# Performance work log

Measured on AMD Instinct MI355X. Metric: run time of the kernel, lower is better.

The kernel has to match this reference:

```python
import jax, jax.numpy as jnp
import numpy as np


def setup_inputs() -> dict:
    key = jax.random.key(0)
    ks = jax.random.split(key, 8)
    N, D, G, H = 131072, 128, 2048, 512
    features = jax.random.normal(ks[0], (N, D), dtype=jnp.float32)
    graph_index = jnp.sort(jax.random.randint(ks[1], (N,), 0, G))
    s1 = 1.0 / np.sqrt(D)
    W_m = jax.random.uniform(ks[2], (H, D), jnp.float32, -s1, s1)
    b_m = jax.random.uniform(ks[3], (H,), jnp.float32, -s1, s1)
    s2 = 1.0 / np.sqrt(H)
    W_ih = jax.random.uniform(ks[4], (4 * H, 2 * H), jnp.float32, -s2, s2)
    W_hh = jax.random.uniform(ks[5], (4 * H, H), jnp.float32, -s2, s2)
    b_ih = jax.random.uniform(ks[6], (4 * H,), jnp.float32, -s2, s2)
    b_hh = jax.random.uniform(ks[7], (4 * H,), jnp.float32, -s2, s2)
    return dict(features=features, graph_index=graph_index, W_m=W_m, b_m=b_m,
                W_ih=W_ih, W_hh=W_hh, b_ih=b_ih, b_hh=b_hh, num_graphs=G)


def reference(features, graph_index, W_m, b_m, W_ih, W_hh, b_ih, b_hh, num_graphs):
    H = W_m.shape[0]
    LOOP = 3
    EPS = 1e-7
    NEG_BIG = -1e10
    m = features @ W_m.T + b_m                      # [N, H]
    h = jnp.zeros((num_graphs, H), m.dtype)
    c = jnp.zeros((num_graphs, H), m.dtype)
    q_star = jnp.zeros((num_graphs, 2 * H), m.dtype)
    for _ in range(LOOP):
        # PyTorch LSTMCell: gates in (i, f, g, o) order
        gates = q_star @ W_ih.T + h @ W_hh.T + (b_ih + b_hh)   # [G, 4H]
        i_g, f_g, g_g, o_g = jnp.split(gates, 4, axis=-1)
        c = jax.nn.sigmoid(f_g) * c + jax.nn.sigmoid(i_g) * jnp.tanh(g_g)
        h = jax.nn.sigmoid(o_g) * jnp.tanh(c)
        # attention scores per node against its graph's query h
        e = jnp.sum(m * h[graph_index], axis=-1, keepdims=True)  # [N, 1]
        e_max = jax.ops.segment_max(e, graph_index, num_segments=num_graphs)
        e_max = jax.lax.stop_gradient(
            jnp.where(jnp.isfinite(e_max), e_max, NEG_BIG))
        e = e - e_max[graph_index]
        exp_e = jnp.exp(jnp.clip(e, -30.0, 20.0))
        exp_sum = jax.ops.segment_sum(exp_e, graph_index, num_segments=num_graphs)
        a = exp_e / (exp_sum[graph_index] + EPS)                 # [N, 1]
        r = jax.ops.segment_sum(m * a, graph_index, num_segments=num_graphs)  # [G, H]
        q_star = jnp.concatenate([h, r], axis=-1)                # [G, 2H]
    return q_star
```

## Files before the change

kernel.cpp:

```cpp
#include <hip/hip_runtime.h>

#define N_NODES 131072
#define DIM     128
#define NG      2048
#define HD      512

typedef unsigned short u16;
typedef _Float16 half8 __attribute__((ext_vector_type(8)));
typedef float  f32x4  __attribute__((ext_vector_type(4)));

__device__ u16   g_wm[(size_t)HD * DIM];
__device__ u16   g_wmT[(size_t)DIM * HD];
__device__ u16   g_wgf[(size_t)2048 * 640];
__device__ u16   g_wih2[(size_t)2048 * 512];
__device__ float g_bc[2048];
__device__ float g_bf[2048];
__device__ float g_gh[2048];
__device__ float g_c0[512];
__device__ float g_w20[128];
__device__ float g_w2[(size_t)NG * DIM];
__device__ float g_tp[NG];
__device__ u16   g_Acat[(size_t)NG * 640];
__device__ u16   g_h3[(size_t)NG * HD];
__device__ float g_c[(size_t)NG * HD];
__device__ int   g_start[NG + 1];
__device__ int   g_isbf16;
__device__ int   g_idx64;

__device__ __forceinline__ float bf2f(u16 u) {
  unsigned v = ((unsigned)u) << 16;
  float f; __builtin_memcpy(&f, &v, 4); return f;
}
__device__ __forceinline__ float u2f_hi(unsigned u) {
  unsigned v = u & 0xFFFF0000u;
  float f; __builtin_memcpy(&f, &v, 4); return f;
}
__device__ __forceinline__ float u2f_lo(unsigned u) {
  unsigned v = u << 16;
  float f; __builtin_memcpy(&f, &v, 4); return f;
}
__device__ __forceinline__ u16 f2bf(float f) {
  unsigned u; __builtin_memcpy(&u, &f, 4);
  u += 0x7FFFu + ((u >> 16) & 1u);
  return (u16)(u >> 16);
}
__device__ __forceinline__ u16 f2h(float f) {
  _Float16 h = (_Float16)f; u16 u; __builtin_memcpy(&u, &h, 2); return u;
}
__device__ __forceinline__ float h2f(u16 u) {
  _Float16 h; __builtin_memcpy(&h, &u, 2); return (float)h;
}
__device__ __forceinline__ float rdf(const void* p, int i) {
  return g_isbf16 ? bf2f(((const u16*)p)[i]) : ((const float*)p)[i];
}
__device__ __forceinline__ float rdl(const void* p, int i, int isb) {
  return isb ? bf2f(((const u16*)p)[i]) : ((const float*)p)[i];
}

#define GLD16(gp, lp) __builtin_amdgcn_global_load_lds(                          \
    (const __attribute__((address_space(1))) void*)(gp),                         \
    (__attribute__((address_space(3))) void*)(lp), 16, 0, 0)

#define NWP ((size_t)HD * DIM / 2)
#define NWT ((size_t)DIM * HD / 2)
#define NW1 ((size_t)2048 * 512 / 2)
#define NW2 ((size_t)2048 * 512 / 2)
#define W_PAIRS (NWP + NWT + NW1 + NW2)

__global__ __launch_bounds__(256) void k_s0(const void* feat, const void* gidxv,
                                            const void* wmp, const void* wih,
                                            const void* whh) {
  __shared__ int s_cnt;
  const int t = threadIdx.x;
  if (t == 0) s_cnt = 0;
  __syncthreads();
  {
    u16 u = ((const u16*)feat)[t];
    float v = bf2f(u);
    float a = fabsf(v);
    int ok = (v == v) && a >= 1e-6f && a <= 1e6f;
    atomicAdd(&s_cnt, ok);
  }
  __syncthreads();
  const int isb = (s_cnt >= 230);
  const int idx64 = (((const int*)gidxv)[N_NODES - 1] == 0);
  if (blockIdx.x == 0 && t == 0) { g_isbf16 = isb; g_idx64 = idx64; }

  for (size_t i = (size_t)blockIdx.x * 256 + t; i < W_PAIRS;
       i += (size_t)gridDim.x * 256) {
    if (i < NWP) {
      float v0, v1;
      if (isb) {
        unsigned pr = ((const unsigned*)wmp)[i];
        v0 = bf2f((u16)pr); v1 = bf2f((u16)(pr >> 16));
      } else {
        float2 v = ((const float2*)wmp)[i];
        v0 = v.x; v1 = v.y;
      }
      ((unsigned*)g_wm)[i] = (unsigned)f2h(v0) | ((unsigned)f2h(v1) << 16);
    } else if (i < NWP + NWT) {
      size_t p = i - NWP;
      int d = (int)(p >> 8), j = (int)(p & 255) * 2;
      float v0 = rdl(wmp, j * DIM + d, isb);
      float v1 = rdl(wmp, (j + 1) * DIM + d, isb);
      ((unsigned*)g_wmT)[(size_t)d * 256 + (j >> 1)] =
          (unsigned)f2h(v0) | ((unsigned)f2h(v1) << 16);
    } else if (i < NWP + NWT + NW1) {
      size_t p = i - NWP - NWT;
      int n = (int)(p >> 8), kp = (int)(p & 255), k = kp * 2;
      int orig = (n & 3) * 512 + (n >> 2);
      float v0 = rdl(wih, orig * 1024 + k, isb)     + rdl(whh, orig * 512 + k, isb);
      float v1 = rdl(wih, orig * 1024 + k + 1, isb) + rdl(whh, orig * 512 + k + 1, isb);
      ((unsigned*)g_wgf)[(size_t)n * 320 + kp] =
          (unsigned)f2h(v0) | ((unsigned)f2h(v1) << 16);
    } else {
      size_t p = i - NWP - NWT - NW1;
      int n = (int)(p >> 8), kp = (int)(p & 255), k = kp * 2;
      int orig = (n & 3) * 512 + (n >> 2);
      float v0 = rdl(wih, orig * 1024 + 512 + k, isb);
      float v1 = rdl(wih, orig * 1024 + 512 + k + 1, isb);
      ((unsigned*)g_wih2)[(size_t)n * 256 + kp] =
          (unsigned)f2h(v0) | ((unsigned)f2h(v1) << 16);
    }
  }
  if (blockIdx.x < 512) {
    int n = blockIdx.x * 256 + t;
    int gg = idx64 ? (int)((const long long*)gidxv)[n] : ((const int*)gidxv)[n];
    if (n == 0) {
      for (int x = 0; x <= gg; ++x) g_start[x] = 0;
    } else {
      int gp = idx64 ? (int)((const long long*)gidxv)[n - 1] : ((const int*)gidxv)[n - 1];
      for (int x = gp + 1; x <= gg; ++x) g_start[x] = n;
    }
    if (n == N_NODES - 1) {
      for (int x = gg + 1; x <= NG; ++x) g_start[x] = N_NODES;
    }
  }
}

__global__ __launch_bounds__(256) void k_s1(const void* bih, const void* bhh,
                                            const void* bm) {
  alignas(16) __shared__ char smem[16384];
  const int t = threadIdx.x, b = blockIdx.x;
  if (b < 128) {
    float* s_bm = (float*)smem;
    float* s_h0 = s_bm + 512;
    for (int p = t; p < 512; p += 256) {
      s_bm[p] = rdf(bm, p);
      float xi = rdf(bih, p)        + rdf(bhh, p);
      float xg = rdf(bih, p + 1024) + rdf(bhh, p + 1024);
      float xo = rdf(bih, p + 1536) + rdf(bhh, p + 1536);
      float si = 1.f / (1.f + __expf(-xi));
      float tg = tanhf(xg);
      float so = 1.f / (1.f + __expf(-xo));
      s_h0[p] = so * tanhf(si * tg);
    }
    __syncthreads();
    const int rloc = t >> 4, k = t & 15;
    const int n = b * 16 + rloc;
    float sbf = 0.f, sgh = 0.f;
#pragma unroll
    for (int j = 0; j < 4; ++j) {
      const int e = k * 8 + j * 128;
      half8 w2v = *(const half8*)(g_wih2 + (size_t)n * 512 + e);
      half8 w1v = *(const half8*)(g_wgf  + (size_t)n * 640 + e);
#pragma unroll
      for (int d = 0; d < 8; ++d) {
        sbf += (float)w2v[d] * s_bm[e + d];
        sgh += (float)w1v[d] * s_h0[e + d];
      }
    }
#pragma unroll
    for (int o = 1; o < 16; o <<= 1) {
      sbf += __shfl_xor(sbf, o, 64);
      sgh += __shfl_xor(sgh, o, 64);
    }
    if (k == 0) {
      const int orig = (n & 3) * 512 + (n >> 2);
      g_bf[n] = sbf;
      g_gh[n] = sgh;
      g_bc[n] = rdf(bih, orig) + rdf(bhh, orig);
    }
  } else if (b < 192) {
    u16* As = (u16*)smem;
    u16* Bs = As + 4096;
    const int bx = b - 128;
    const int lid = t & 63, w = t >> 6;
    const int m0 = (bx & 31) * 64, n0 = (bx >> 5) * 64;
    const int rr = lid & 15, quad = lid >> 4;
    const int rsub = lid >> 3;
    const int cs = (lid & 7) ^ rsub;
    const int wm = (w >> 1) * 32, wn = (w & 1) * 32;
    f32x4 acc[2][2] = {};
    for (int kt = 0; kt < 8; ++kt) {
      const int k0 = kt * 64;
      GLD16(g_wih2 + (size_t)(m0 + w * 16 + rsub) * 512 + k0 + cs * 8, As + (w * 16) * 64);
      GLD16(g_wih2 + (size_t)(m0 + w * 16 + 8 + rsub) * 512 + k0 + cs * 8, As + (w * 16 + 8) * 64);
      GLD16(g_wmT + (size_t)(n0 + w * 16 + rsub) * 512 + k0 + cs * 8, Bs + (w * 16) * 64);
      GLD16(g_wmT + (size_t)(n0 + w * 16 + 8 + rsub) * 512 + k0 + cs * 8, Bs + (w * 16 + 8) * 64);
      __syncthreads();
#pragma unroll
      for (int kk = 0; kk < 2; ++kk) {
        const int qb = kk * 4 + quad;
        const int sw = (qb ^ (rr & 7)) << 3;
        half8 af[2], bfr[2];
#pragma unroll
        for (int i = 0; i < 2; ++i) af[i]  = *(const half8*)(As + (wm + i * 16 + rr) * 64 + sw);
#pragma unroll
        for (int j = 0; j < 2; ++j) bfr[j] = *(const half8*)(Bs + (wn + j * 16 + rr) * 64 + sw);
#pragma unroll
        for (int i = 0; i < 2; ++i)
#pragma unroll
          for (int j = 0; j < 2; ++j)
            acc[i][j] = __builtin_amdgcn_mfma_f32_16x16x32_f16(bfr[j], af[i], acc[i][j], 0, 0, 0);
      }
      __syncthreads();
    }
#pragma unroll
    for (int i = 0; i < 2; ++i)
#pragma unroll
      for (int j = 0; j < 2; ++j) {
        const int row = m0 + wm + i * 16 + rr;
        const int c0 = n0 + wn + j * 16 + quad * 4;
        u16 h4[4];
#pragma unroll
        for (int r = 0; r < 4; ++r) h4[r] = f2h(acc[i][j][r]);
        *(uint2*)(g_wgf + (size_t)row * 640 + 512 + c0) =
            make_uint2((unsigned)h4[0] | ((unsigned)h4[1] << 16),
                       (unsigned)h4[2] | ((unsigned)h4[3] << 16));
      }
  } else if (b == 192) {
    float* s_h   = (float*)smem;
    float* s_red = s_h + 512;
    for (int j = t; j < 512; j += 256) {
      float xi = rdf(bih, j)        + rdf(bhh, j);
      float xg = rdf(bih, j + 1024) + rdf(bhh, j + 1024);
      float xo = rdf(bih, j + 1536) + rdf(bhh, j + 1536);
      float si = 1.f / (1.f + __expf(-xi));
      float tg = tanhf(xg);
      float so = 1.f / (1.f + __expf(-xo));
      float cn = si * tg;
      float hn = so * tanhf(cn);
      g_c0[j] = cn;
      s_h[j] = hn;
    }
    __syncthreads();
    const int dg = t & 15, jg = t >> 4;
    float a8[8] = {};
    for (int jj = 0; jj < 32; ++jj) {
      const int j = jg * 32 + jj;
      half8 wv = *(const half8*)(g_wm + (size_t)j * 128 + dg * 8);
      const float hv = s_h[j];
#pragma unroll
      for (int d = 0; d < 8; ++d) a8[d] += hv * (float)wv[d];
    }
#pragma unroll
    for (int d = 0; d < 8; ++d) {
      a8[d] += __shfl_xor(a8[d], 16, 64);
      a8[d] += __shfl_xor(a8[d], 32, 64);
    }
    const int w = t >> 6;
    if ((t & 63) < 16) {
      *(f32x4*)&s_red[w * 128 + dg * 8]     = *(f32x4*)&a8[0];
      *(f32x4*)&s_red[w * 128 + dg * 8 + 4] = *(f32x4*)&a8[4];
    }
    __syncthreads();
    if (t < 128)
      g_w20[t] = s_red[t] + s_red[128 + t] + s_red[256 + t] + s_red[384 + t];
  }
}

__global__ __launch_bounds__(256) void k_w2(int hsel) {
  alignas(16) __shared__ u16 As[64 * 64];
  alignas(16) __shared__ u16 Bs[64 * 64];
  const int t = threadIdx.x, lid = t & 63, w = t >> 6;
  const int m0 = blockIdx.x * 64, n0 = blockIdx.y * 64;
  const int rr = lid & 15, quad = lid >> 4;
  const int rsub = lid >> 3;
  const int cs = (lid & 7) ^ rsub;
  const int wm = (w >> 1) * 32, wn = (w & 1) * 32;
  const u16* Ap = hsel ? g_h3 : g_Acat;
  const int astr = hsel ? 512 : 640;
  f32x4 acc[2][2] = {};
  for (int kt = 0; kt < 8; ++kt) {
    const int k0 = kt * 64;
    GLD16(Ap + (size_t)(m0 + w * 16 + rsub) * astr + k0 + cs * 8, As + (w * 16) * 64);
    GLD16(Ap + (size_t)(m0 + w * 16 + 8 + rsub) * astr + k0 + cs * 8, As + (w * 16 + 8) * 64);
    GLD16(g_wmT + (size_t)(n0 + w * 16 + rsub) * 512 + k0 + cs * 8, Bs + (w * 16) * 64);
    GLD16(g_wmT + (size_t)(n0 + w * 16 + 8 + rsub) * 512 + k0 + cs * 8, Bs + (w * 16 + 8) * 64);
    __syncthreads();
#pragma unroll
    for (int kk = 0; kk < 2; ++kk) {
      const int qb = kk * 4 + quad;
      const int sw = (qb ^ (rr & 7)) << 3;
      half8 af[2], bfr[2];
#pragma unroll
      for (int i = 0; i < 2; ++i) af[i]  = *(const half8*)(As + (wm + i * 16 + rr) * 64 + sw);
#pragma unroll
      for (int j = 0; j < 2; ++j) bfr[j] = *(const half8*)(Bs + (wn + j * 16 + rr) * 64 + sw);
#pragma unroll
      for (int i = 0; i < 2; ++i)
#pragma unroll
        for (int j = 0; j < 2; ++j)
          acc[i][j] = __builtin_amdgcn_mfma_f32_16x16x32_f16(bfr[j], af[i], acc[i][j], 0, 0, 0);
    }
    __syncthreads();
  }
#pragma unroll
  for (int i = 0; i < 2; ++i)
#pragma unroll
    for (int j = 0; j < 2; ++j) {
      const int row = m0 + wm + i * 16 + rr;
      const int c0 = n0 + wn + j * 16 + quad * 4;
      *(f32x4*)(g_w2 + (size_t)row * DIM + c0) = acc[i][j];
    }
}

__global__ __launch_bounds__(256) void k_gemm(int ktiles2, int aoff, int useGh,
                                              int first, int wout, int h3out,
                                              void* __restrict__ out) {
  alignas(16) __shared__ u16 As[2][64 * 64];
  alignas(16) __shared__ u16 Bs[2][64 * 64];
  const int t = threadIdx.x, lid = t & 63, w = t >> 6;
  const int m0 = (blockIdx.x & 31) * 64, n0 = (blockIdx.x >> 5) * 64;
  const int rr = lid & 15, quad = lid >> 4;
  const int rsub = lid >> 3;
  const int cs = (lid & 7) ^ rsub;
  const int wm = (w >> 1) * 32, wn = (w & 1) * 32;
  const int isb = g_isbf16;
  f32x4 acc[2][2] = {};
  for (int kt2 = 0; kt2 < ktiles2; ++kt2) {
#pragma unroll
    for (int b = 0; b < 2; ++b) {
      const int k0 = aoff + (kt2 * 2 + b) * 64;
      GLD16(g_Acat + (size_t)(m0 + w * 16 + rsub) * 640 + k0 + cs * 8, As[b] + (w * 16) * 64);
      GLD16(g_Acat + (size_t)(m0 + w * 16 + 8 + rsub) * 640 + k0 + cs * 8, As[b] + (w * 16 + 8) * 64);
      GLD16(g_wgf  + (size_t)(n0 + w * 16 + rsub) * 640 + k0 + cs * 8, Bs[b] + (w * 16) * 64);
      GLD16(g_wgf  + (size_t)(n0 + w * 16 + 8 + rsub) * 640 + k0 + cs * 8, Bs[b] + (w * 16 + 8) * 64);
    }
    __syncthreads();
#pragma unroll
    for (int b = 0; b < 2; ++b)
#pragma unroll
      for (int kk = 0; kk < 2; ++kk) {
        const int qb = kk * 4 + quad;
        const int sw = (qb ^ (rr & 7)) << 3;
        half8 af[2], bfr[2];
#pragma unroll
        for (int i = 0; i < 2; ++i) af[i]  = *(const half8*)(As[b] + (wm + i * 16 + rr) * 64 + sw);
#pragma unroll
        for (int j = 0; j < 2; ++j) bfr[j] = *(const half8*)(Bs[b] + (wn + j * 16 + rr) * 64 + sw);
#pragma unroll
        for (int i = 0; i < 2; ++i)
#pragma unroll
          for (int j = 0; j < 2; ++j)
            acc[i][j] = __builtin_amdgcn_mfma_f32_16x16x32_f16(bfr[j], af[i], acc[i][j], 0, 0, 0);
      }
    __syncthreads();
  }
#pragma unroll
  for (int i = 0; i < 2; ++i) {
    const int row = m0 + wm + i * 16 + rr;
    const float tp = g_tp[row];
#pragma unroll
    for (int j = 0; j < 2; ++j) {
      const int c0 = n0 + wn + j * 16 + quad * 4;
      const int jj = c0 >> 2;
      float4 bc = *(const float4*)(g_bc + c0);
      float4 bf = *(const float4*)(g_bf + c0);
      float gx = 0.f, gy = 0.f, gz = 0.f, gw = 0.f;
      if (useGh) {
        float4 gh = *(const float4*)(g_gh + c0);
        gx = gh.x; gy = gh.y; gz = gh.z; gw = gh.w;
      }
      float xi = acc[i][j][0] + bc.x + gx + tp * bf.x;
      float xf = acc[i][j][1] + bc.y + gy + tp * bf.y;
      float xg = acc[i][j][2] + bc.z + gz + tp * bf.z;
      float xo = acc[i][j][3] + bc.w + gw + tp * bf.w;
      float si = 1.f / (1.f + __expf(-xi));
      float sf = 1.f / (1.f + __expf(-xf));
      float tg = tanhf(xg);
      float so = 1.f / (1.f + __expf(-xo));
      float cp = first ? g_c0[jj] : g_c[(size_t)row * 512 + jj];
      float cn = sf * cp + si * tg;
      float hn = so * tanhf(cn);
      g_c[(size_t)row * 512 + jj] = cn;
      if (h3out) g_h3[(size_t)row * 512 + jj] = f2h(hn);
      else       g_Acat[(size_t)row * 640 + jj] = f2h(hn);
      if (wout) {
        if (isb) ((u16*)out)[(size_t)row * 1024 + jj] = f2bf(hn);
        else     ((float*)out)[(size_t)row * 1024 + jj] = hn;
      }
    }
  }
}

__global__ __launch_bounds__(256) void k_attn(const void* __restrict__ feat,
                                              int w2sel, int fin,
                                              void* __restrict__ out,
                                              const void* __restrict__ bm) {
  __shared__ float s_m[4], s_l[4];
  __shared__ float s_s[4][DIM];
  __shared__ float s_keep[DIM];
  __shared__ float s_tpv[1];
  const int g = blockIdx.x;
  const int t = threadIdx.x, lid = t & 63, wid = t >> 6;
  const int c = lid & 15;
  const int slot = lid >> 4;
  const int israw = g_isbf16;
  const int s = g_start[g], e = g_start[g + 1];
  float w2r[8];
  if (w2sel) {
    *(float4*)(w2r)     = *(const float4*)(g_w2 + (size_t)g * DIM + c * 8);
    *(float4*)(w2r + 4) = *(const float4*)(g_w2 + (size_t)g * DIM + c * 8 + 4);
  } else {
    *(float4*)(w2r)     = *(const float4*)(g_w20 + c * 8);
    *(float4*)(w2r + 4) = *(const float4*)(g_w20 + c * 8 + 4);
  }
  float mrun = -3.0e38f, lsum = 0.f;
  float racc[8] = {0.f, 0.f, 0.f, 0.f, 0.f, 0.f, 0.f, 0.f};
  for (int nb = s + wid * 4; nb < e; nb += 16) {
    const int n = nb + slot;
    float fv[8], d;
    if (n < e) {
      if (israw) {
        uint4 q = *(const uint4*)((const u16*)feat + (size_t)n * DIM + c * 8);
        fv[0] = u2f_lo(q.x); fv[1] = u2f_hi(q.x);
        fv[2] = u2f_lo(q.y); fv[3] = u2f_hi(q.y);
        fv[4] = u2f_lo(q.z); fv[5] = u2f_hi(q.z);
        fv[6] = u2f_lo(q.w); fv[7] = u2f_hi(q.w);
      } else {
        const float* fp = (const float*)feat + (size_t)n * DIM + c * 8;
        float4 f0 = *(const float4*)fp;
        float4 f1 = *(const float4*)(fp + 4);
        fv[0] = f0.x; fv[1] = f0.y; fv[2] = f0.z; fv[3] = f0.w;
        fv[4] = f1.x; fv[5] = f1.y; fv[6] = f1.z; fv[7] = f1.w;
      }
      d = 0.f;
#pragma unroll
      for (int j = 0; j < 8; ++j) d += fv[j] * w2r[j];
    } else {
      d = -1.0e30f;
#pragma unroll
      for (int j = 0; j < 8; ++j) fv[j] = 0.f;
    }
#pragma unroll
    for (int o = 1; o < 16; o <<= 1) d += __shfl_xor(d, o, 64);
    float m4 = fmaxf(d, __shfl_xor(d, 16, 64));
    m4 = fmaxf(m4, __shfl_xor(m4, 32, 64));
    float mnew = fmaxf(mrun, m4);
    float sc = __expf(mrun - mnew);
    float w = __expf(d - mnew);
    lsum = lsum * sc + w;
#pragma unroll
    for (int j = 0; j < 8; ++j) racc[j] = racc[j] * sc + w * fv[j];
    mrun = mnew;
  }
  float lt = lsum + __shfl_xor(lsum, 16, 64);
  lt += __shfl_xor(lt, 32, 64);
#pragma unroll
  for (int j = 0; j < 8; ++j) {
    racc[j] += __shfl_xor(racc[j], 16, 64);
    racc[j] += __shfl_xor(racc[j], 32, 64);
  }
  if (lid == 0) s_m[wid] = mrun;
  __syncthreads();
  float gmax = fmaxf(fmaxf(s_m[0], s_m[1]), fmaxf(s_m[2], s_m[3]));
  float scw = __expf(mrun - gmax);
  if (lid < 16) {
    float4 lo = make_float4(racc[0] * scw, racc[1] * scw, racc[2] * scw, racc[3] * scw);
    float4 hi = make_float4(racc[4] * scw, racc[5] * scw, racc[6] * scw, racc[7] * scw);
    *(f32x4*)&s_s[wid][c * 8] = *(f32x4*)&lo;
    *(f32x4*)&s_s[wid][c * 8 + 4] = *(f32x4*)&hi;
  }
  if (lid == 0) s_l[wid] = lt * scw;
  __syncthreads();
  float total = s_l[0] + s_l[1] + s_l[2] + s_l[3];
  float inv = 1.f / (total + 1e-7f);
  if (!fin) {
    if (t == 0) g_tp[g] = total * inv;
    if (t < 64) {
      int d0 = t * 2;
      float v0 = (s_s[0][d0] + s_s[1][d0] + s_s[2][d0] + s_s[3][d0]) * inv;
      float v1 = (s_s[0][d0 + 1] + s_s[1][d0 + 1] + s_s[2][d0 + 1] + s_s[3][d0 + 1]) * inv;
      ((unsigned*)g_Acat)[(size_t)g * 320 + 256 + t] =
          (unsigned)f2h(v0) | ((unsigned)f2h(v1) << 16);
    }
  } else {
    if (t == 0) s_tpv[0] = total * inv;
    if (t < 64) {
      int d0 = t * 2;
      s_keep[d0]     = (s_s[0][d0] + s_s[1][d0] + s_s[2][d0] + s_s[3][d0]) * inv;
      s_keep[d0 + 1] = (s_s[0][d0 + 1] + s_s[1][d0 + 1] + s_s[2][d0 + 1] + s_s[3][d0 + 1]) * inv;
    }
    __syncthreads();
    const int jj = t * 2;
    const unsigned* wt = (const unsigned*)g_wmT;
    float a0 = 0.f, a1 = 0.f;
#pragma unroll 8
    for (int d = 0; d < 128; ++d) {
      unsigned pr = wt[d * 256 + t];
      float kv = s_keep[d];
      a0 += kv * h2f((u16)pr);
      a1 += kv * h2f((u16)(pr >> 16));
    }
    float tp = s_tpv[0];
    float r0 = a0 + tp * rdf(bm, jj);
    float r1 = a1 + tp * rdf(bm, jj + 1);
    if (israw) {
      ((unsigned*)out)[((size_t)g * 1024 + 512 + jj) >> 1] =
          (unsigned)f2bf(r0) | ((unsigned)f2bf(r1) << 16);
    } else {
      *(float2*)((float*)out + (size_t)g * 1024 + 512 + jj) = make_float2(r0, r1);
    }
  }
}

extern "C" void kernel_launch(void* const* d_in, const int* in_sizes, int n_in,
                              void* d_out, int out_size, void* d_ws, size_t ws_size,
                              hipStream_t stream) {
  const void* features = d_in[0];
  const void* gidx     = d_in[1];
  const void* W_m      = d_in[2];
  const void* b_m      = d_in[3];
  const void* W_ih     = d_in[4];
  const void* W_hh     = d_in[5];
  const void* b_ih     = d_in[6];
  const void* b_hh     = d_in[7];

  k_s0<<<1024, 256, 0, stream>>>(features, gidx, W_m, W_ih, W_hh);
  k_s1<<<193, 256, 0, stream>>>(b_ih, b_hh, b_m);
  k_attn<<<NG, 256, 0, stream>>>(features, 0, 0, d_out, b_m);
  k_gemm<<<1024, 256, 0, stream>>>(1, 512, 1, 1, 0, 0, d_out);
  k_w2<<<dim3(32, 2), 256, 0, stream>>>(0);
  k_attn<<<NG, 256, 0, stream>>>(features, 1, 0, d_out, b_m);
  k_gemm<<<1024, 256, 0, stream>>>(5, 0, 0, 0, 1, 1, d_out);
  k_w2<<<dim3(32, 2), 256, 0, stream>>>(1);
  k_attn<<<NG, 256, 0, stream>>>(features, 1, 1, d_out, b_m);
}
```

Measured before the change: 213.4 us.

## Move final r projection to MFMA GEMM kernel and widen LSTM gate tiles

The final attention pass no longer does a scalar per-block 128x512 projection through W_m^T. It now writes the pooled features to Acat, and a separate MFMA GEMM kernel (k_r) computes r = pooled·W_m^T + tp·b_m. Separately, the gate GEMM tile grows from 64x64 to 64x128 per block, halving the grid and reusing A fragments across more MFMAs. This adds one kernel launch and more LDS per gate-GEMM block, which may lower occupancy.

```diff
diff --git a/kernel.cpp b/kernel.cpp
--- a/kernel.cpp
+++ b/kernel.cpp
@@ -320,23 +320,25 @@
                                               int first, int wout, int h3out,
                                               void* __restrict__ out) {
   alignas(16) __shared__ u16 As[2][64 * 64];
-  alignas(16) __shared__ u16 Bs[2][64 * 64];
+  alignas(16) __shared__ u16 Bs[2][128 * 64];
   const int t = threadIdx.x, lid = t & 63, w = t >> 6;
-  const int m0 = (blockIdx.x & 31) * 64, n0 = (blockIdx.x >> 5) * 64;
+  const int m0 = (blockIdx.x & 31) * 64, n0 = (blockIdx.x >> 5) * 128;
   const int rr = lid & 15, quad = lid >> 4;
   const int rsub = lid >> 3;
   const int cs = (lid & 7) ^ rsub;
-  const int wm = (w >> 1) * 32, wn = (w & 1) * 32;
+  const int wn = w * 32;
   const int isb = g_isbf16;
-  f32x4 acc[2][2] = {};
+  f32x4 acc[4][2] = {};
   for (int kt2 = 0; kt2 < ktiles2; ++kt2) {
 #pragma unroll
     for (int b = 0; b < 2; ++b) {
       const int k0 = aoff + (kt2 * 2 + b) * 64;
       GLD16(g_Acat + (size_t)(m0 + w * 16 + rsub) * 640 + k0 + cs * 8, As[b] + (w * 16) * 64);
       GLD16(g_Acat + (size_t)(m0 + w * 16 + 8 + rsub) * 640 + k0 + cs * 8, As[b] + (w * 16 + 8) * 64);
-      GLD16(g_wgf  + (size_t)(n0 + w * 16 + rsub) * 640 + k0 + cs * 8, Bs[b] + (w * 16) * 64);
-      GLD16(g_wgf  + (size_t)(n0 + w * 16 + 8 + rsub) * 640 + k0 + cs * 8, Bs[b] + (w * 16 + 8) * 64);
+      GLD16(g_wgf + (size_t)(n0 + w * 32 + rsub) * 640 + k0 + cs * 8, Bs[b] + (w * 32) * 64);
+      GLD16(g_wgf + (size_t)(n0 + w * 32 + 8 + rsub) * 640 + k0 + cs * 8, Bs[b] + (w * 32 + 8) * 64);
+      GLD16(g_wgf + (size_t)(n0 + w * 32 + 16 + rsub) * 640 + k0 + cs * 8, Bs[b] + (w * 32 + 16) * 64);
+      GLD16(g_wgf + (size_t)(n0 + w * 32 + 24 + rsub) * 640 + k0 + cs * 8, Bs[b] + (w * 32 + 24) * 64);
     }
     __syncthreads();
 #pragma unroll
@@ -345,13 +347,13 @@
       for (int kk = 0; kk < 2; ++kk) {
         const int qb = kk * 4 + quad;
         const int sw = (qb ^ (rr & 7)) << 3;
-        half8 af[2], bfr[2];
-#pragma unroll
-        for (int i = 0; i < 2; ++i) af[i]  = *(const half8*)(As[b] + (wm + i * 16 + rr) * 64 + sw);
+        half8 af[4], bfr[2];
+#pragma unroll
+        for (int i = 0; i < 4; ++i) af[i]  = *(const half8*)(As[b] + (i * 16 + rr) * 64 + sw);
 #pragma unroll
         for (int j = 0; j < 2; ++j) bfr[j] = *(const half8*)(Bs[b] + (wn + j * 16 + rr) * 64 + sw);
 #pragma unroll
-        for (int i = 0; i < 2; ++i)
+        for (int i = 0; i < 4; ++i)
 #pragma unroll
           for (int j = 0; j < 2; ++j)
             acc[i][j] = __builtin_amdgcn_mfma_f32_16x16x32_f16(bfr[j], af[i], acc[i][j], 0, 0, 0);
@@ -359,8 +361,8 @@
     __syncthreads();
   }
 #pragma unroll
-  for (int i = 0; i < 2; ++i) {
-    const int row = m0 + wm + i * 16 + rr;
+  for (int i = 0; i < 4; ++i) {
+    const int row = m0 + i * 16 + rr;
     const float tp = g_tp[row];
 #pragma unroll
     for (int j = 0; j < 2; ++j) {
@@ -396,13 +398,9 @@
 }
 
 __global__ __launch_bounds__(256) void k_attn(const void* __restrict__ feat,
-                                              int w2sel, int fin,
-                                              void* __restrict__ out,
-                                              const void* __restrict__ bm) {
+                                              int w2sel) {
   __shared__ float s_m[4], s_l[4];
   __shared__ float s_s[4][DIM];
-  __shared__ float s_keep[DIM];
-  __shared__ float s_tpv[1];
   const int g = blockIdx.x;
   const int t = threadIdx.x, lid = t & 63, wid = t >> 6;
   const int c = lid & 15;
@@ -477,41 +475,72 @@
   __syncthreads();
   float total = s_l[0] + s_l[1] + s_l[2] + s_l[3];
   float inv = 1.f / (total + 1e-7f);
-  if (!fin) {
-    if (t == 0) g_tp[g] = total * inv;
-    if (t < 64) {
-      int d0 = t * 2;
-      float v0 = (s_s[0][d0] + s_s[1][d0] + s_s[2][d0] + s_s[3][d0]) * inv;
-      float v1 = (s_s[0][d0 + 1] + s_s[1][d0 + 1] + s_s[2][d0 + 1] + s_s[3][d0 + 1]) * inv;
-      ((unsigned*)g_Acat)[(size_t)g * 320 + 256 + t] =
-          (unsigned)f2h(v0) | ((unsigned)f2h(v1) << 16);
-    }
-  } else {
-    if (t == 0) s_tpv[0] = total * inv;
-    if (t < 64) {
-      int d0 = t * 2;
-      s_keep[d0]     = (s_s[0][d0] + s_s[1][d0] + s_s[2][d0] + s_s[3][d0]) * inv;
-      s_keep[d0 + 1] = (s_s[0][d0 + 1] + s_s[1][d0 + 1] + s_s[2][d0 + 1] + s_s[3][d0 + 1]) * inv;
-    }
-    __syncthreads();
-    const int jj = t * 2;
-    const unsigned* wt = (const unsigned*)g_wmT;
-    float a0 = 0.f, a1 = 0.f;
-#pragma unroll 8
-    for (int d = 0; d < 128; ++d) {
-      unsigned pr = wt[d * 256 + t];
-      float kv = s_keep[d];
-      a0 += kv * h2f((u16)pr);
-      a1 += kv * h2f((u16)(pr >> 16));
-    }
-    float tp = s_tpv[0];
-    float r0 = a0 + tp * rdf(bm, jj);
-    float r1 = a1 + tp * rdf(bm, jj + 1);
-    if (israw) {
-      ((unsigned*)out)[((size_t)g * 1024 + 512 + jj) >> 1] =
-          (unsigned)f2bf(r0) | ((unsigned)f2bf(r1) << 16);
-    } else {
-      *(float2*)((float*)out + (size_t)g * 1024 + 512 + jj) = make_float2(r0, r1);
+  if (t == 0) g_tp[g] = total * inv;
+  if (t < 64) {
+    int d0 = t * 2;
+    float v0 = (s_s[0][d0] + s_s[1][d0] + s_s[2][d0] + s_s[3][d0]) * inv;
+    float v1 = (s_s[0][d0 + 1] + s_s[1][d0 + 1] + s_s[2][d0 + 1] + s_s[3][d0 + 1]) * inv;
+    ((unsigned*)g_Acat)[(size_t)g * 320 + 256 + t] =
+        (unsigned)f2h(v0) | ((unsigned)f2h(v1) << 16);
+  }
+}
+
+__global__ __launch_bounds__(256) void k_r(const void* __restrict__ bias,
+                                           void* __restrict__ out) {
+  alignas(16) __shared__ u16 As[64 * 64];
+  alignas(16) __shared__ u16 Bs[64 * 64];
+  const int t = threadIdx.x, lid = t & 63, w = t >> 6;
+  const int m0 = blockIdx.x * 64, n0 = blockIdx.y * 64;
+  const int rr = lid & 15, quad = lid >> 4;
+  const int rsub = lid >> 3;
+  const int cs = (lid & 7) ^ rsub;
+  const int wm = (w >> 1) * 32, wn = (w & 1) * 32;
+  f32x4 acc[2][2] = {};
+  for (int kt = 0; kt < 2; ++kt) {
+    const int k0 = kt * 64;
+    GLD16(g_Acat + (size_t)(m0 + w * 16 + rsub) * 640 + 512 + k0 + cs * 8, As + (w * 16) * 64);
+    GLD16(g_Acat + (size_t)(m0 + w * 16 + 8 + rsub) * 640 + 512 + k0 + cs * 8, As + (w * 16 + 8) * 64);
+    GLD16(g_wm + (size_t)(n0 + w * 16 + rsub) * 128 + k0 + cs * 8, Bs + (w * 16) * 64);
+    GLD16(g_wm + (size_t)(n0 + w * 16 + 8 + rsub) * 128 + k0 + cs * 8, Bs + (w * 16 + 8) * 64);
+    __syncthreads();
+#pragma unroll
+    for (int kk = 0; kk < 2; ++kk) {
+      const int qb = kk * 4 + quad;
+      const int sw = (qb ^ (rr & 7)) << 3;
+      half8 af[2], bfr[2];
+#pragma unroll
+      for (int i = 0; i < 2; ++i) af[i]  = *(const half8*)(As + (wm + i * 16 + rr) * 64 + sw);
+#pragma unroll
+      for (int j = 0; j < 2; ++j) bfr[j] = *(const half8*)(Bs + (wn + j * 16 + rr) * 64 + sw);
+#pragma unroll
+      for (int i = 0; i < 2; ++i)
+#pragma unroll
+        for (int j = 0; j < 2; ++j)
+          acc[i][j] = __builtin_amdgcn_mfma_f32_16x16x32_f16(bfr[j], af[i], acc[i][j], 0, 0, 0);
+    }
+    __syncthreads();
+  }
+  const int isb = g_isbf16;
+#pragma unroll
+  for (int i = 0; i < 2; ++i) {
+    const int row = m0 + wm + i * 16 + rr;
+    const float tp = g_tp[row];
+#pragma unroll
+    for (int j = 0; j < 2; ++j) {
+      const int c0 = n0 + wn + j * 16 + quad * 4;
+      float rv[4];
+#pragma unroll
+      for (int r = 0; r < 4; ++r) rv[r] = acc[i][j][r] + tp * rdf(bias, c0 + r);
+      if (isb) {
+        u16 b4[4];
+#pragma unroll
+        for (int r = 0; r < 4; ++r) b4[r] = f2bf(rv[r]);
+        *(uint2*)((u16*)out + (size_t)row * 1024 + 512 + c0) =
+            make_uint2((unsigned)b4[0] | ((unsigned)b4[1] << 16),
+                       (unsigned)b4[2] | ((unsigned)b4[3] << 16));
+      } else {
+        *(f32x4*)((float*)out + (size_t)row * 1024 + 512 + c0) = *(f32x4*)rv;
+      }
     }
   }
 }
@@ -530,11 +559,12 @@
 
   k_s0<<<1024, 256, 0, stream>>>(features, gidx, W_m, W_ih, W_hh);
   k_s1<<<193, 256, 0, stream>>>(b_ih, b_hh, b_m);
-  k_attn<<<NG, 256, 0, stream>>>(features, 0, 0, d_out, b_m);
-  k_gemm<<<1024, 256, 0, stream>>>(1, 512, 1, 1, 0, 0, d_out);
+  k_attn<<<NG, 256, 0, stream>>>(features, 0);
+  k_gemm<<<512, 256, 0, stream>>>(1, 512, 1, 1, 0, 0, d_out);
   k_w2<<<dim3(32, 2), 256, 0, stream>>>(0);
-  k_attn<<<NG, 256, 0, stream>>>(features, 1, 0, d_out, b_m);
-  k_gemm<<<1024, 256, 0, stream>>>(5, 0, 0, 0, 1, 1, d_out);
+  k_attn<<<NG, 256, 0, stream>>>(features, 1);
+  k_gemm<<<512, 256, 0, stream>>>(5, 0, 0, 0, 1, 1, d_out);
   k_w2<<<dim3(32, 2), 256, 0, stream>>>(1);
-  k_attn<<<NG, 256, 0, stream>>>(features, 1, 1, d_out, b_m);
-}
+  k_attn<<<NG, 256, 0, stream>>>(features, 1);
+  k_r<<<dim3(32, 8), 256, 0, stream>>>(b_m, d_out);
+}
```

Result: no change. 212.6 us (-0.4%).
